# Kernel tuning notes

Hardware: AMD Instinct MI355X
Metric: run time of the kernel (lower is better)

The kernel has to match this reference:

```python
import jax, jax.numpy as jnp
import numpy as np

EPS = 1e-5  # torch LayerNorm default

def _ln(x, g, b):
    mu = jnp.mean(x, -1, keepdims=True)
    var = jnp.mean((x - mu) ** 2, -1, keepdims=True)
    return (x - mu) * jax.lax.rsqrt(var + EPS) * g + b

def _xavier(key, shape):
    fan_in, fan_out = shape[-2], shape[-1]
    s = (2.0 / (fan_in + fan_out)) ** 0.5
    return jax.random.normal(key, shape, dtype=jnp.float32) * s

def setup_inputs() -> dict:
    key = jax.random.key(0)
    ks = jax.random.split(key, 24)
    N, E, B = 10000, 160000, 64
    D, M, FF, K = 128, 32, 32, 5
    EIN = 2 * FF + 1 + 2 * D          # 321
    inp = {}
    inp["coords"] = jax.random.normal(ks[0], (N, 3), dtype=jnp.float32)
    inp["atomids"] = jax.random.randint(ks[1], (N,), 0, 11)
    inp["edge_index"] = jax.random.randint(ks[2], (2, E), 0, N)
    inp["batch"] = jnp.sort(jax.random.randint(ks[3], (N,), 0, B))
    inp["num_graphs"] = B
    inp["emb"] = _xavier(ks[4], (11, D))
    # stacked per-kernel EGNN params (leading dim K=5)
    inp["keW1"] = _xavier(ks[5], (K, EIN, 2 * EIN)); inp["keb1"] = jnp.zeros((K, 2 * EIN))
    inp["keW2"] = _xavier(ks[6], (K, 2 * EIN, M));   inp["keb2"] = jnp.zeros((K, M))
    inp["keng"] = jnp.ones((K, M));   inp["kenb"] = jnp.zeros((K, M))
    inp["kn1g"] = jnp.ones((K, D));   inp["kn1b"] = jnp.zeros((K, D))
    inp["knW1"] = _xavier(ks[7], (K, D + M, 2 * D)); inp["knb1"] = jnp.zeros((K, 2 * D))
    inp["knW2"] = _xavier(ks[8], (K, 2 * D, D));     inp["knb2"] = jnp.zeros((K, D))
    inp["kn2g"] = jnp.ones((K, D));   inp["kn2b"] = jnp.zeros((K, D))
    # fnn: (K+1)*D = 768 -> 256 -> 256 -> 256
    inp["fW0"] = _xavier(ks[9], ((K + 1) * D, 256)); inp["fb0"] = jnp.zeros((256,))
    inp["fW1"] = _xavier(ks[10], (256, 256));        inp["fb1"] = jnp.zeros((256,))
    inp["fW2"] = _xavier(ks[11], (256, 256));        inp["fb2"] = jnp.zeros((256,))
    # fnn2: 256 -> 256 -> 256 -> 1
    inp["gW0"] = _xavier(ks[12], (256, 256));        inp["gb0"] = jnp.zeros((256,))
    inp["gW1"] = _xavier(ks[13], (256, 256));        inp["gb1"] = jnp.zeros((256,))
    inp["gW2"] = _xavier(ks[14], (256, 1));          inp["gb2"] = jnp.zeros((1,))
    return inp

def reference(coords, atomids, edge_index, batch, num_graphs, emb,
              keW1, keb1, keW2, keb2, keng, kenb, kn1g, kn1b,
              knW1, knb1, knW2, knb2, kn2g, kn2b,
              fW0, fb0, fW1, fb1, fW2, fb2,
              gW0, gb0, gW1, gb1, gW2, gb2):
    silu = jax.nn.silu
    N = coords.shape[0]
    src, dst = edge_index[0], edge_index[1]  # x_j = x[src], x_i = x[dst]
    feats = emb[atomids]                                  # [N,128]
    # coords are never updated across kernels -> fourier edge attr computed once
    rel = coords[src] - coords[dst]                       # [E,3]
    d = jnp.sum(rel * rel, -1, keepdims=True)             # [E,1] squared distance
    scales = 2.0 ** jnp.arange(32, dtype=coords.dtype)
    xs = d / scales                                       # [E,32]
    ea = jnp.concatenate([jnp.sin(xs), jnp.cos(xs), d], -1)  # [E,65]
    ones_e = jnp.ones((src.shape[0], 1), feats.dtype)
    deg = jax.ops.segment_sum(ones_e, dst, num_segments=N)   # [N,1]
    deg = jnp.maximum(deg, 1.0)
    feat_list = [feats]
    for k in range(keW1.shape[0]):
        # edge message MLP
        m = jnp.concatenate([feats[dst], feats[src], ea], -1)        # [E,321]
        h = silu(m @ keW1[k] + keb1[k])                              # [E,642]
        m_ij = silu(h @ keW2[k] + keb2[k])                           # [E,32]
        m_ij = _ln(m_ij, keng[k], kenb[k])
        # scatter-mean aggregate to target nodes
        m_i = jax.ops.segment_sum(m_ij, dst, num_segments=N) / deg   # [N,32]
        m_i = _ln(m_i, keng[k], kenb[k])  # (original reuses edge_norm1)
        # node update MLP with residual
        hf = _ln(feats, kn1g[k], kn1b[k])
        h2 = silu(jnp.concatenate([hf, m_i], -1) @ knW1[k] + knb1[k])
        h2 = h2 @ knW2[k] + knb2[k]
        h2 = _ln(h2, kn2g[k], kn2b[k])
        feats = feats + h2
        feat_list.append(feats)
    f = silu(jnp.concatenate(feat_list, -1))              # [N,768]
    f = silu(f @ fW0 + fb0)
    f = silu(f @ fW1 + fb1)
    f = silu(f @ fW2 + fb2)
    gs = jax.ops.segment_sum(f, batch, num_segments=num_graphs)
    gc = jax.ops.segment_sum(jnp.ones((N, 1), f.dtype), batch, num_segments=num_graphs)
    g = gs / jnp.maximum(gc, 1.0)                         # [B,256] scatter_mean
    g = silu(g @ gW0 + gb0)
    g = silu(g @ gW1 + gb1)
    return g @ gW2 + gb2                                  # [B,1]
```

## Files before the change

### kernel.cpp

```cpp
#include <hip/hip_runtime.h>
#include <cstdint>
#include <cstddef>


#define DEV __device__ __forceinline__

typedef __attribute__((ext_vector_type(8))) short bf16x8;
typedef __attribute__((ext_vector_type(4))) float f32x4;

DEV float siluf(float x) { return x / (1.f + __expf(-x)); }

DEV unsigned short f2bf(float f) {
  unsigned u = __float_as_uint(f);
  unsigned r = u + 0x7FFFu + ((u >> 16) & 1u);
  return (unsigned short)(r >> 16);
}
DEV float bf2f(unsigned short h) { return __uint_as_float(((unsigned)h) << 16); }

DEV f32x4 mfma16(bf16x8 a, bf16x8 b, f32x4 c) {
  return __builtin_amdgcn_mfma_f32_16x16x32_bf16(a, b, c, 0, 0, 0);
}

DEV void unpack8(bf16x8 v, float* o) {
#pragma unroll
  for (int j = 0; j < 8; ++j) o[j] = bf2f((unsigned short)v[j]);
}

__global__ __launch_bounds__(256) void k_gather(const int* __restrict__ atomids,
                                                const float* __restrict__ emb,
                                                float* __restrict__ feats_all,
                                                unsigned short* __restrict__ fH, int N) {
  int idx = blockIdx.x * 256 + threadIdx.x;
  if (idx >= N * 128) return;
  int i = idx >> 7, j = idx & 127;
  float v = emb[atomids[i] * 128 + j];
  size_t o = (size_t)i * 768 + j;
  feats_all[o] = v;
  fH[o] = f2bf(v);
}

__global__ __launch_bounds__(256) void k_edge_prep(const float* __restrict__ coords,
                                                   const int* __restrict__ ei, int E,
                                                   float* __restrict__ d_arr,
                                                   int* __restrict__ cnt) {
  int e = blockIdx.x * 256 + threadIdx.x;
  if (e >= E) return;
  int s = ei[e], t = ei[E + e];
  float dx = coords[3 * s + 0] - coords[3 * t + 0];
  float dy = coords[3 * s + 1] - coords[3 * t + 1];
  float dz = coords[3 * s + 2] - coords[3 * t + 2];
  d_arr[e] = dx * dx + dy * dy + dz * dz;
  atomicAdd(&cnt[t], 1);
}

__global__ __launch_bounds__(1024) void k_scan(const int* __restrict__ cnt, int N,
                                               int* __restrict__ cursor,
                                               float* __restrict__ degf) {
  __shared__ int s[1024];
  __shared__ int carry;
  if (threadIdx.x == 0) carry = 0;
  __syncthreads();
  for (int base = 0; base < N; base += 1024) {
    int i = base + threadIdx.x;
    int v = (i < N) ? cnt[i] : 0;
    s[threadIdx.x] = v;
    __syncthreads();
    for (int off = 1; off < 1024; off <<= 1) {
      int add = (threadIdx.x >= off) ? s[threadIdx.x - off] : 0;
      __syncthreads();
      s[threadIdx.x] += add;
      __syncthreads();
    }
    if (i < N) {
      cursor[i] = s[threadIdx.x] - v + carry;
      degf[i] = fmaxf((float)v, 1.f);
    }
    __syncthreads();
    if (threadIdx.x == 0) carry += s[1023];
    __syncthreads();
  }
}

__global__ __launch_bounds__(256) void k_scatter(const int* __restrict__ ei, int E,
                                                 const float* __restrict__ d_arr,
                                                 int* __restrict__ cursor,
                                                 int* __restrict__ ssrc,
                                                 int* __restrict__ sdst,
                                                 float* __restrict__ sd) {
  int e = blockIdx.x * 256 + threadIdx.x;
  if (e >= E) return;
  int s = ei[e], t = ei[E + e];
  int p = atomicAdd(&cursor[t], 1);
  ssrc[p] = s;
  sdst[p] = t;
  sd[p] = d_arr[e];
}

__global__ __launch_bounds__(256) void k_prepack(
    const float* __restrict__ W, size_t wStride, int ldw,
    int K, int Kpad, int Ncols, int Npad,
    unsigned short* __restrict__ hi, unsigned short* __restrict__ lo, size_t oStride) {
  int idx = blockIdx.x * 256 + threadIdx.x;
  int total = Npad * Kpad;
  if (idx >= total) return;
  W += blockIdx.y * wStride;
  hi += blockIdx.y * oStride;
  lo += blockIdx.y * oStride;
  int n = idx / Kpad, k = idx - n * Kpad;
  float v = (n < Ncols && k < K) ? W[(size_t)k * ldw + n] : 0.f;
  unsigned short h = f2bf(v);
  hi[idx] = h;
  lo[idx] = f2bf(v - bf2f(h));
}

__global__ __launch_bounds__(256) void gemm_bf(
    const unsigned short* __restrict__ AH, int lda,
    const unsigned short* __restrict__ BH, const unsigned short* __restrict__ BL, int ldb,
    const float* __restrict__ bias,
    float* __restrict__ C, int ldc,
    unsigned short* __restrict__ CH, int ldch, int outPlaneN,
    int M, int Ncols, int K, int actOut, int actA) {
  const int t = threadIdx.x;
  const int wave = t >> 6, lane = t & 63;
  const int nl = lane & 15, quad = lane >> 4;
  const int bm = blockIdx.x * 128 + wave * 32;
  const int bn = blockIdx.y * 64;
  f32x4 zero = {0.f, 0.f, 0.f, 0.f};
  f32x4 acc[2][4] = {{zero, zero, zero, zero}, {zero, zero, zero, zero}};
  for (int kb = 0; kb < K; kb += 32) {
    bf16x8 ah[2];
#pragma unroll
    for (int h = 0; h < 2; ++h) {
      int row = bm + h * 16 + nl;
      if (row < M) {
        ah[h] = *(const bf16x8*)(AH + (size_t)row * lda + kb + quad * 8);
        if (actA) {
#pragma unroll
          for (int j = 0; j < 8; ++j) {
            float a = siluf(bf2f((unsigned short)ah[h][j]));
            ah[h][j] = (short)f2bf(a);
          }
        }
      } else {
#pragma unroll
        for (int j = 0; j < 8; ++j) ah[h][j] = 0;
      }
    }
#pragma unroll
    for (int tn = 0; tn < 4; ++tn) {
      size_t boff = (size_t)(bn + tn * 16 + nl) * ldb + kb + quad * 8;
      bf16x8 bh = *(const bf16x8*)(BH + boff);
      bf16x8 bl = *(const bf16x8*)(BL + boff);
#pragma unroll
      for (int h = 0; h < 2; ++h) {
        acc[h][tn] = mfma16(ah[h], bh, acc[h][tn]);
        acc[h][tn] = mfma16(ah[h], bl, acc[h][tn]);
      }
    }
  }
#pragma unroll
  for (int h = 0; h < 2; ++h) {
#pragma unroll
    for (int tn = 0; tn < 4; ++tn) {
      int c = bn + tn * 16 + nl;
      float bv = (bias && c < Ncols) ? bias[c] : 0.f;
#pragma unroll
      for (int r = 0; r < 4; ++r) {
        int rr = bm + h * 16 + quad * 4 + r;
        if (rr >= M) continue;
        float v = acc[h][tn][r] + bv;
        if (actOut) v = siluf(v);
        if (C && c < Ncols) C[(size_t)rr * ldc + c] = v;
        if (CH) {
          unsigned short us = f2bf(v);
          if (outPlaneN > 0)
            CH[(size_t)blockIdx.y * outPlaneN + (size_t)rr * 64 + tn * 16 + nl] = us;
          else if (c < Ncols)
            CH[(size_t)rr * ldch + c] = us;
        }
      }
    }
  }
}

__global__ __launch_bounds__(256, 3) void k_edge_mfma(
    const unsigned short* __restrict__ Ap, const unsigned short* __restrict__ Bp,
    int planeN,
    const int* __restrict__ ssrc, const int* __restrict__ sdst,
    const float* __restrict__ sd_g, int E,
    const unsigned short* __restrict__ WeaT,
    const float* __restrict__ Wea64,
    const unsigned short* __restrict__ W2T,
    const float* __restrict__ b2v,
    const float* __restrict__ eng, const float* __restrict__ enb,
    float* __restrict__ msum) {
  __shared__ float sAB[4][16 * 68];
  __shared__ float sH[4][16 * 68];
  __shared__ float sDs[64];
  __shared__ int sSrcS[64], sDstS[64];

  const int t = threadIdx.x;
  const int wave = t >> 6, lane = t & 63;
  const int nl = lane & 15, quad = lane >> 4;
  const int e0 = blockIdx.x * 64;

  if (lane < 16) {
    int el = wave * 16 + lane;
    int e = e0 + el;
    int ec = (e < E) ? e : (E - 1);
    sSrcS[el] = ssrc[ec];
    sDstS[el] = sdst[ec];
    sDs[el] = sd_g[ec];
  }
  const int r = lane >> 2, cq = lane & 3;
  const int elr = wave * 16 + r;
  const size_t aOff = (size_t)sDstS[elr] * 64 + cq * 16;
  const size_t bOff = (size_t)sSrcS[elr] * 64 + cq * 16;
  const float dR = sDs[elr];
  float* myAB = sAB[wave];
  float* myH = sH[wave];

  bf16x8 pa0, pa1, pb0, pb1;
  bf16x8 w1[4][2], w2a[2][2], w2b[2][2];

  auto loadW1 = [&](int c) {
#pragma unroll
    for (int tn = 0; tn < 4; ++tn)
#pragma unroll
      for (int ks = 0; ks < 2; ++ks)
        w1[tn][ks] = *(const bf16x8*)(WeaT + (size_t)(c * 64 + tn * 16 + nl) * 64 +
                                      ks * 32 + quad * 8);
  };
  auto loadW2 = [&](int c, bf16x8(*w)[2]) {
#pragma unroll
    for (int tn = 0; tn < 2; ++tn)
#pragma unroll
      for (int ks = 0; ks < 2; ++ks)
        w[tn][ks] = *(const bf16x8*)(W2T + (size_t)(tn * 16 + nl) * 704 + c * 64 +
                                     ks * 32 + quad * 8);
  };
  auto issue = [&](int c) {
    const unsigned short* a = Ap + (size_t)c * planeN + aOff;
    const unsigned short* b = Bp + (size_t)c * planeN + bOff;
    pa0 = *(const bf16x8*)a;
    pa1 = *(const bf16x8*)(a + 8);
    pb0 = *(const bf16x8*)b;
    pb1 = *(const bf16x8*)(b + 8);
  };
  auto commit = [&](int c) {
    float za[16], zb[16], w[16];
    unpack8(pa0, za); unpack8(pa1, za + 8);
    unpack8(pb0, zb); unpack8(pb1, zb + 8);
    const int cb = c * 64 + cq * 16;
    if (cb + 15 < 642) {
#pragma unroll
      for (int j = 0; j < 4; ++j) {
        f32x4 wv = *(const f32x4*)(Wea64 + cb + 4 * j);
        w[4 * j] = wv.x; w[4 * j + 1] = wv.y; w[4 * j + 2] = wv.z; w[4 * j + 3] = wv.w;
      }
    } else {
#pragma unroll
      for (int u = 0; u < 16; ++u) w[u] = (cb + u < 642) ? Wea64[cb + u] : 0.f;
    }
#pragma unroll
    for (int j = 0; j < 4; ++j) {
      f32x4 o;
#pragma unroll
      for (int u = 0; u < 4; ++u) o[u] = za[4 * j + u] + zb[4 * j + u] + dR * w[4 * j + u];
      *(f32x4*)(myAB + r * 68 + cq * 16 + 4 * j) = o;
    }
  };

  issue(0);
  bf16x8 eaHi[2];
  {
    float d = sDs[wave * 16 + nl];
#pragma unroll
    for (int ks = 0; ks < 2; ++ks)
#pragma unroll
      for (int j = 0; j < 8; ++j) {
        int k = ks * 32 + quad * 8 + j;
        float arg = d * exp2f(-(float)(k & 31));
        float v = (k < 32) ? __sinf(arg) : __cosf(arg);
        eaHi[ks][j] = (short)f2bf(v);
      }
  }
  loadW1(0);
  loadW2(0, w2a);

  f32x4 zero = {0.f, 0.f, 0.f, 0.f};
  f32x4 macc[2] = {zero, zero};

#pragma unroll
  for (int c = 0; c < 11; ++c) {
    commit(c);
    if (c < 10) issue(c + 1);
    f32x4 acc1[4] = {zero, zero, zero, zero};
#pragma unroll
    for (int tn = 0; tn < 4; ++tn)
#pragma unroll
      for (int ks = 0; ks < 2; ++ks) acc1[tn] = mfma16(eaHi[ks], w1[tn][ks], acc1[tn]);
#pragma unroll
    for (int tn = 0; tn < 4; ++tn)
#pragma unroll
      for (int rr = 0; rr < 4; ++rr) {
        int lrow = quad * 4 + rr;
        float z = acc1[tn][rr] + myAB[lrow * 68 + tn * 16 + nl];
        myH[lrow * 68 + tn * 16 + nl] = siluf(z);
      }
    if (c < 10) {
      loadW1(c + 1);
      loadW2(c + 1, (c & 1) ? w2a : w2b);
    }
    bf16x8(*w2)[2] = (c & 1) ? w2b : w2a;
#pragma unroll
    for (int ks = 0; ks < 2; ++ks) {
      f32x4 h0 = *(const f32x4*)(myH + nl * 68 + ks * 32 + quad * 8);
      f32x4 h1 = *(const f32x4*)(myH + nl * 68 + ks * 32 + quad * 8 + 4);
      bf16x8 ah;
      ah[0] = (short)f2bf(h0.x); ah[1] = (short)f2bf(h0.y);
      ah[2] = (short)f2bf(h0.z); ah[3] = (short)f2bf(h0.w);
      ah[4] = (short)f2bf(h1.x); ah[5] = (short)f2bf(h1.y);
      ah[6] = (short)f2bf(h1.z); ah[7] = (short)f2bf(h1.w);
#pragma unroll
      for (int tn = 0; tn < 2; ++tn) macc[tn] = mfma16(ah, w2[tn][ks], macc[tn]);
    }
  }

  float g0 = eng[nl], g1v = eng[16 + nl], bb0 = enb[nl], bb1 = enb[16 + nl];
  float bi0 = b2v[nl], bi1 = b2v[16 + nl];
  float* sMw = myH;
#pragma unroll
  for (int rr = 0; rr < 4; ++rr) {
    float v0 = siluf(macc[0][rr] + bi0);
    float v1 = siluf(macc[1][rr] + bi1);
    float s = v0 + v1;
    float ss = v0 * v0 + v1 * v1;
#pragma unroll
    for (int m = 1; m < 16; m <<= 1) {
      s += __shfl_xor(s, m, 16);
      ss += __shfl_xor(ss, m, 16);
    }
    float mu = s * (1.f / 32.f);
    float var = ss * (1.f / 32.f) - mu * mu;
    float rs = rsqrtf(var + 1e-5f);
    int lr = quad * 4 + rr;
    sMw[lr * 33 + nl] = (v0 - mu) * rs * g0 + bb0;
    sMw[lr * 33 + 16 + nl] = (v1 - mu) * rs * g1v + bb1;
  }
  __syncthreads();
  {
    int col = t & 31, seg = t >> 5;
    float acc = 0.f;
    int cur = -1;
#pragma unroll
    for (int i = 0; i < 8; ++i) {
      int e = seg * 8 + i;
      int dn = (e0 + e < E) ? sDstS[e] : -1;
      if (dn != cur) {
        if (cur >= 0) atomicAdd(&msum[(size_t)cur * 32 + col], acc);
        acc = 0.f;
        cur = dn;
      }
      if (dn >= 0) acc += sH[e >> 4][(e & 15) * 33 + col];
    }
    if (cur >= 0) atomicAdd(&msum[(size_t)cur * 32 + col], acc);
  }
}

__global__ __launch_bounds__(256) void k_node_ln(
    const float* __restrict__ msum, const float* __restrict__ deg,
    const float* __restrict__ featsAll, int k,
    const float* __restrict__ n1g, const float* __restrict__ n1b,
    const float* __restrict__ eng, const float* __restrict__ enb,
    unsigned short* __restrict__ hcatH, int N) {
  int node = blockIdx.x * 4 + (threadIdx.x >> 6);
  int lane = threadIdx.x & 63;
  if (node >= N) return;
  const float* fr = featsAll + (size_t)node * 768 + k * 128;
  float x0 = fr[lane], x1 = fr[64 + lane];
  float s = x0 + x1;
#pragma unroll
  for (int m = 1; m < 64; m <<= 1) s += __shfl_xor(s, m, 64);
  float mu = s * (1.f / 128.f);
  float d0 = x0 - mu, d1 = x1 - mu;
  float v = d0 * d0 + d1 * d1;
#pragma unroll
  for (int m = 1; m < 64; m <<= 1) v += __shfl_xor(v, m, 64);
  float rstd = rsqrtf(v * (1.f / 128.f) + 1e-5f);
  size_t hb = (size_t)node * 160;
  hcatH[hb + lane] = f2bf(d0 * rstd * n1g[lane] + n1b[lane]);
  hcatH[hb + 64 + lane] = f2bf(d1 * rstd * n1g[64 + lane] + n1b[64 + lane]);
  float dg = deg[node];
  int col = lane & 31;
  float y = msum[(size_t)node * 32 + col] / dg;
  float sy = y;
#pragma unroll
  for (int m = 1; m < 32; m <<= 1) sy += __shfl_xor(sy, m, 32);
  float mu2 = sy * (1.f / 32.f);
  float dy = y - mu2;
  float vy = dy * dy;
#pragma unroll
  for (int m = 1; m < 32; m <<= 1) vy += __shfl_xor(vy, m, 32);
  float rstd2 = rsqrtf(vy * (1.f / 32.f) + 1e-5f);
  if (lane < 32) hcatH[hb + 128 + col] = f2bf(dy * rstd2 * eng[col] + enb[col]);
}

__global__ __launch_bounds__(256) void k_node_resid(
    const float* __restrict__ t2, float* __restrict__ featsAll, int k,
    const float* __restrict__ n2g, const float* __restrict__ n2b,
    unsigned short* __restrict__ fH, int N) {
  int node = blockIdx.x * 4 + (threadIdx.x >> 6);
  int lane = threadIdx.x & 63;
  if (node >= N) return;
  const float* tr = t2 + (size_t)node * 128;
  float x0 = tr[lane], x1 = tr[64 + lane];
  float s = x0 + x1;
#pragma unroll
  for (int m = 1; m < 64; m <<= 1) s += __shfl_xor(s, m, 64);
  float mu = s * (1.f / 128.f);
  float d0 = x0 - mu, d1 = x1 - mu;
  float v = d0 * d0 + d1 * d1;
#pragma unroll
  for (int m = 1; m < 64; m <<= 1) v += __shfl_xor(v, m, 64);
  float rstd = rsqrtf(v * (1.f / 128.f) + 1e-5f);
  const float* fk = featsAll + (size_t)node * 768 + k * 128;
  size_t ob = (size_t)node * 768 + (k + 1) * 128;
  float o0 = fk[lane] + d0 * rstd * n2g[lane] + n2b[lane];
  float o1 = fk[64 + lane] + d1 * rstd * n2g[64 + lane] + n2b[64 + lane];
  featsAll[ob + lane] = o0;
  featsAll[ob + 64 + lane] = o1;
  fH[ob + lane] = f2bf(o0);
  fH[ob + 64 + lane] = f2bf(o1);
}

__global__ __launch_bounds__(256) void k_pool2(const float* __restrict__ f,
                                               const int* __restrict__ batch,
                                               float* __restrict__ gsum,
                                               float* __restrict__ gcnt, int N) {
  int n0 = blockIdx.x * 64;
  int col = threadIdx.x;
  float acc = 0.f;
  int cur = -1;
  for (int i = 0; i < 64; ++i) {
    int n = n0 + i;
    if (n >= N) break;
    int b = batch[n];
    if (b != cur) {
      if (cur >= 0) atomicAdd(&gsum[cur * 256 + col], acc);
      acc = 0.f;
      cur = b;
    }
    acc += f[(size_t)n * 256 + col];
  }
  if (cur >= 0) atomicAdd(&gsum[cur * 256 + col], acc);
  if (threadIdx.x == 0) {
    int cnt = 0;
    cur = -1;
    for (int i = 0; i < 64; ++i) {
      int n = n0 + i;
      if (n >= N) break;
      int b = batch[n];
      if (b != cur) {
        if (cur >= 0) atomicAdd(&gcnt[cur], (float)cnt);
        cnt = 0;
        cur = b;
      }
      cnt++;
    }
    if (cur >= 0) atomicAdd(&gcnt[cur], (float)cnt);
  }
}

__global__ void k_gdiv(float* gsum, const float* gcnt, unsigned short* gH) {
  int b = blockIdx.x, j = threadIdx.x;
  float v = gsum[b * 256 + j] / fmaxf(gcnt[b], 1.f);
  gH[b * 256 + j] = f2bf(v);
}

__global__ void k_gout(const float* __restrict__ g2, const float* __restrict__ gW2,
                       const float* __restrict__ gb2, float* __restrict__ out) {
  int b = threadIdx.x;
  if (b >= 64) return;
  float s = gb2[0];
  for (int j = 0; j < 256; ++j) s += g2[b * 256 + j] * gW2[j];
  out[b] = s;
}

extern "C" void kernel_launch(void* const* d_in, const int* in_sizes, int n_in,
                              void* d_out, int out_size, void* d_ws, size_t ws_size,
                              hipStream_t stream) {
  const float* coords = (const float*)d_in[0];
  const int* atomids = (const int*)d_in[1];
  const int* ei = (const int*)d_in[2];
  const int* batch = (const int*)d_in[3];
  const float* emb = (const float*)d_in[5];
  const float* keW1 = (const float*)d_in[6];
  const float* keb1 = (const float*)d_in[7];
  const float* keW2 = (const float*)d_in[8];
  const float* keb2 = (const float*)d_in[9];
  const float* keng = (const float*)d_in[10];
  const float* kenb = (const float*)d_in[11];
  const float* kn1g = (const float*)d_in[12];
  const float* kn1b = (const float*)d_in[13];
  const float* knW1 = (const float*)d_in[14];
  const float* knb1 = (const float*)d_in[15];
  const float* knW2 = (const float*)d_in[16];
  const float* knb2 = (const float*)d_in[17];
  const float* kn2g = (const float*)d_in[18];
  const float* kn2b = (const float*)d_in[19];
  const float* fW0 = (const float*)d_in[20];
  const float* fb0 = (const float*)d_in[21];
  const float* fW1 = (const float*)d_in[22];
  const float* fb1 = (const float*)d_in[23];
  const float* fW2 = (const float*)d_in[24];
  const float* fb2 = (const float*)d_in[25];
  const float* gW0 = (const float*)d_in[26];
  const float* gb0 = (const float*)d_in[27];
  const float* gW1 = (const float*)d_in[28];
  const float* gb1 = (const float*)d_in[29];
  const float* gW2 = (const float*)d_in[30];
  const float* gb2 = (const float*)d_in[31];

  const int N = in_sizes[0] / 3;
  const int E = in_sizes[2] / 2;
  const int planeN = N * 64;

  size_t off = 0;
  auto alloc = [&](size_t n) {
    float* p = (float*)d_ws + off;
    off += (n + 63) & ~(size_t)63;
    return p;
  };
  float* feats_all = alloc((size_t)N * 768);
  float* d_arr = alloc(E);
  float* degf = alloc(N);
  float* msum = alloc((size_t)N * 32);
  float* t2 = alloc((size_t)N * 128);
  float* f1 = alloc((size_t)N * 256);
  float* gsum = alloc(64 * 256);
  float* gcnt = alloc(64);
  float* g2 = alloc(64 * 256);
  int* cnt = (int*)alloc(N);
  int* cursor = (int*)alloc(N);
  int* ssrc = (int*)alloc(E);
  int* sdst = (int*)alloc(E);
  float* sd = alloc(E);

  unsigned short* ubase = (unsigned short*)(alloc(0));
  size_t uoff = 0;
  auto ualloc = [&](size_t n) {
    unsigned short* p = ubase + uoff;
    uoff += (n + 63) & ~(size_t)63;
    return p;
  };
  unsigned short* fH = ualloc((size_t)N * 768);
  unsigned short* ApU = ualloc((size_t)11 * planeN);
  unsigned short* BpU = ualloc((size_t)11 * planeN);
  unsigned short* hcatH = ualloc((size_t)N * 160);
  unsigned short* t1H = ualloc((size_t)N * 256);
  unsigned short* fAH = ualloc((size_t)N * 256);
  unsigned short* fBH = ualloc((size_t)N * 256);
  unsigned short* gH = ualloc(64 * 256);
  unsigned short* g1H = ualloc(64 * 256);
  const size_t sDst_ = 704 * 128, sSrc_ = 704 * 128, sEa_ = 704 * 64;
  const size_t sW2_ = 32 * 704, sN1_ = 256 * 160, sN2_ = 128 * 256;
  unsigned short* PdstH = ualloc(5 * sDst_); unsigned short* PdstL = ualloc(5 * sDst_);
  unsigned short* PsrcH = ualloc(5 * sSrc_); unsigned short* PsrcL = ualloc(5 * sSrc_);
  unsigned short* PeaH = ualloc(5 * sEa_);   unsigned short* PeaL = ualloc(5 * sEa_);
  unsigned short* PW2H = ualloc(5 * sW2_);   unsigned short* PW2L = ualloc(5 * sW2_);
  unsigned short* Pn1H = ualloc(5 * sN1_);   unsigned short* Pn1L = ualloc(5 * sN1_);
  unsigned short* Pn2H = ualloc(5 * sN2_);   unsigned short* Pn2L = ualloc(5 * sN2_);
  unsigned short* Pf0H = ualloc(256 * 768);  unsigned short* Pf0L = ualloc(256 * 768);
  unsigned short* Pf1H = ualloc(256 * 256);  unsigned short* Pf1L = ualloc(256 * 256);
  unsigned short* Pf2H = ualloc(256 * 256);  unsigned short* Pf2L = ualloc(256 * 256);
  unsigned short* Pg0H = ualloc(256 * 256);  unsigned short* Pg0L = ualloc(256 * 256);
  unsigned short* Pg1H = ualloc(256 * 256);  unsigned short* Pg1L = ualloc(256 * 256);

  auto pp = [&](const float* W, size_t wStr, int ldw, int K, int Kpad, int Nc, int Npad,
                unsigned short* hi, unsigned short* lo, size_t oStr, int layers) {
    int total = Npad * Kpad;
    k_prepack<<<dim3((total + 255) / 256, layers), 256, 0, stream>>>(
        W, wStr, ldw, K, Kpad, Nc, Npad, hi, lo, oStr);
  };
  pp(keW1, (size_t)321 * 642, 642, 128, 128, 642, 704, PdstH, PdstL, sDst_, 5);
  pp(keW1 + 128 * 642, (size_t)321 * 642, 642, 128, 128, 642, 704, PsrcH, PsrcL, sSrc_, 5);
  pp(keW1 + 256 * 642, (size_t)321 * 642, 642, 64, 64, 642, 704, PeaH, PeaL, sEa_, 5);
  pp(keW2, (size_t)642 * 32, 32, 642, 704, 32, 32, PW2H, PW2L, sW2_, 5);
  pp(knW1, (size_t)160 * 256, 256, 160, 160, 256, 256, Pn1H, Pn1L, sN1_, 5);
  pp(knW2, (size_t)256 * 128, 128, 256, 256, 128, 128, Pn2H, Pn2L, sN2_, 5);
  pp(fW0, 0, 256, 768, 768, 256, 256, Pf0H, Pf0L, 0, 1);
  pp(fW1, 0, 256, 256, 256, 256, 256, Pf1H, Pf1L, 0, 1);
  pp(fW2, 0, 256, 256, 256, 256, 256, Pf2H, Pf2L, 0, 1);
  pp(gW0, 0, 256, 256, 256, 256, 256, Pg0H, Pg0L, 0, 1);
  pp(gW1, 0, 256, 256, 256, 256, 256, Pg1H, Pg1L, 0, 1);

  k_gather<<<(N * 128 + 255) / 256, 256, 0, stream>>>(atomids, emb, feats_all, fH, N);
  hipMemsetAsync(cnt, 0, (size_t)N * sizeof(int), stream);
  k_edge_prep<<<(E + 255) / 256, 256, 0, stream>>>(coords, ei, E, d_arr, cnt);
  k_scan<<<1, 1024, 0, stream>>>(cnt, N, cursor, degf);
  k_scatter<<<(E + 255) / 256, 256, 0, stream>>>(ei, E, d_arr, cursor, ssrc, sdst, sd);

  const int MT = (N + 127) / 128;
  for (int k = 0; k < 5; ++k) {
    gemm_bf<<<dim3(MT, 11), 256, 0, stream>>>(
        fH + k * 128, 768, PdstH + k * sDst_, PdstL + k * sDst_, 128,
        keb1 + k * 642, nullptr, 0, ApU, 0, planeN, N, 642, 128, 0, 0);
    gemm_bf<<<dim3(MT, 11), 256, 0, stream>>>(
        fH + k * 128, 768, PsrcH + k * sSrc_, PsrcL + k * sSrc_, 128,
        nullptr, nullptr, 0, BpU, 0, planeN, N, 642, 128, 0, 0);
    hipMemsetAsync(msum, 0, (size_t)N * 32 * sizeof(float), stream);
    k_edge_mfma<<<(E + 63) / 64, 256, 0, stream>>>(
        ApU, BpU, planeN, ssrc, sdst, sd, E,
        PeaH + k * sEa_,
        keW1 + (size_t)k * 321 * 642 + (size_t)320 * 642,
        PW2H + k * sW2_,
        keb2 + k * 32, keng + k * 32, kenb + k * 32, msum);
    k_node_ln<<<(N + 3) / 4, 256, 0, stream>>>(
        msum, degf, feats_all, k, kn1g + k * 128, kn1b + k * 128,
        keng + k * 32, kenb + k * 32, hcatH, N);
    gemm_bf<<<dim3(MT, 4), 256, 0, stream>>>(
        hcatH, 160, Pn1H + k * sN1_, Pn1L + k * sN1_, 160,
        knb1 + k * 256, nullptr, 0, t1H, 256, 0, N, 256, 160, 1, 0);
    gemm_bf<<<dim3(MT, 2), 256, 0, stream>>>(
        t1H, 256, Pn2H + k * sN2_, Pn2L + k * sN2_, 256,
        knb2 + k * 128, t2, 128, nullptr, 0, 0, N, 128, 256, 0, 0);
    k_node_resid<<<(N + 3) / 4, 256, 0, stream>>>(
        t2, feats_all, k, kn2g + k * 128, kn2b + k * 128, fH, N);
  }

  gemm_bf<<<dim3(MT, 4), 256, 0, stream>>>(
      fH, 768, Pf0H, Pf0L, 768, fb0, nullptr, 0, fAH, 256, 0, N, 256, 768, 1, 1);
  gemm_bf<<<dim3(MT, 4), 256, 0, stream>>>(
      fAH, 256, Pf1H, Pf1L, 256, fb1, nullptr, 0, fBH, 256, 0, N, 256, 256, 1, 0);
  gemm_bf<<<dim3(MT, 4), 256, 0, stream>>>(
      fBH, 256, Pf2H, Pf2L, 256, fb2, f1, 256, nullptr, 0, 0, N, 256, 256, 1, 0);

  hipMemsetAsync(gsum, 0, 64 * 256 * sizeof(float), stream);
  hipMemsetAsync(gcnt, 0, 64 * sizeof(float), stream);
  k_pool2<<<(N + 63) / 64, 256, 0, stream>>>(f1, batch, gsum, gcnt, N);
  k_gdiv<<<64, 256, 0, stream>>>(gsum, gcnt, gH);
  gemm_bf<<<dim3(1, 4), 256, 0, stream>>>(
      gH, 256, Pg0H, Pg0L, 256, gb0, nullptr, 0, g1H, 256, 0, 64, 256, 256, 1, 0);
  gemm_bf<<<dim3(1, 4), 256, 0, stream>>>(
      g1H, 256, Pg1H, Pg1L, 256, gb1, g2, 256, nullptr, 0, 0, 64, 256, 256, 1, 0);
  k_gout<<<1, 64, 0, stream>>>(g2, gW2, gb2, (float*)d_out);
}
```

Baseline: 1.868 ms.

## Merge dst/src projection GEMMs and slim edge kernel registers and LDS

```diff
diff --git a/kernel.cpp b/kernel.cpp
--- a/kernel.cpp
+++ b/kernel.cpp
@@ -118,7 +118,7 @@
     const unsigned short* __restrict__ BH, const unsigned short* __restrict__ BL, int ldb,
     const float* __restrict__ bias,
     float* __restrict__ C, int ldc,
-    unsigned short* __restrict__ CH, int ldch, int outPlaneN,
+    unsigned short* __restrict__ CH, int ldch,
     int M, int Ncols, int K, int actOut, int actA) {
   const int t = threadIdx.x;
   const int wave = t >> 6, lane = t & 63;
@@ -171,19 +171,75 @@
         float v = acc[h][tn][r] + bv;
         if (actOut) v = siluf(v);
         if (C && c < Ncols) C[(size_t)rr * ldc + c] = v;
-        if (CH) {
-          unsigned short us = f2bf(v);
-          if (outPlaneN > 0)
-            CH[(size_t)blockIdx.y * outPlaneN + (size_t)rr * 64 + tn * 16 + nl] = us;
-          else if (c < Ncols)
-            CH[(size_t)rr * ldch + c] = us;
-        }
-      }
-    }
-  }
-}
-
-__global__ __launch_bounds__(256, 3) void k_edge_mfma(
+        if (CH && c < Ncols) CH[(size_t)rr * ldch + c] = f2bf(v);
+      }
+    }
+  }
+}
+
+__global__ __launch_bounds__(256) void gemm_proj(
+    const unsigned short* __restrict__ AH, int lda,
+    const unsigned short* __restrict__ B1H, const unsigned short* __restrict__ B1L,
+    const unsigned short* __restrict__ B2H, const unsigned short* __restrict__ B2L,
+    const float* __restrict__ bias1,
+    unsigned short* __restrict__ C1, unsigned short* __restrict__ C2,
+    int planeN, int M) {
+  const int y = blockIdx.y;
+  const unsigned short* BH;
+  const unsigned short* BL;
+  const float* bias;
+  unsigned short* CP;
+  int yp;
+  if (y < 11) { BH = B1H; BL = B1L; bias = bias1; CP = C1; yp = y; }
+  else        { BH = B2H; BL = B2L; bias = nullptr; CP = C2; yp = y - 11; }
+  const int t = threadIdx.x;
+  const int wave = t >> 6, lane = t & 63;
+  const int nl = lane & 15, quad = lane >> 4;
+  const int bm = blockIdx.x * 128 + wave * 32;
+  const int bn = yp * 64;
+  f32x4 zero = {0.f, 0.f, 0.f, 0.f};
+  f32x4 acc[2][4] = {{zero, zero, zero, zero}, {zero, zero, zero, zero}};
+  for (int kb = 0; kb < 128; kb += 32) {
+    bf16x8 ah[2];
+#pragma unroll
+    for (int h = 0; h < 2; ++h) {
+      int row = bm + h * 16 + nl;
+      if (row < M)
+        ah[h] = *(const bf16x8*)(AH + (size_t)row * lda + kb + quad * 8);
+      else
+#pragma unroll
+        for (int j = 0; j < 8; ++j) ah[h][j] = 0;
+    }
+#pragma unroll
+    for (int tn = 0; tn < 4; ++tn) {
+      size_t boff = (size_t)(bn + tn * 16 + nl) * 128 + kb + quad * 8;
+      bf16x8 bh = *(const bf16x8*)(BH + boff);
+      bf16x8 bl = *(const bf16x8*)(BL + boff);
+#pragma unroll
+      for (int h = 0; h < 2; ++h) {
+        acc[h][tn] = mfma16(ah[h], bh, acc[h][tn]);
+        acc[h][tn] = mfma16(ah[h], bl, acc[h][tn]);
+      }
+    }
+  }
+#pragma unroll
+  for (int h = 0; h < 2; ++h) {
+#pragma unroll
+    for (int tn = 0; tn < 4; ++tn) {
+      int c = bn + tn * 16 + nl;
+      float bv = (bias && c < 642) ? bias[c] : 0.f;
+#pragma unroll
+      for (int r = 0; r < 4; ++r) {
+        int rr = bm + h * 16 + quad * 4 + r;
+        if (rr >= M) continue;
+        CP[(size_t)yp * planeN + (size_t)rr * 64 + tn * 16 + nl] =
+            f2bf(acc[h][tn][r] + bv);
+      }
+    }
+  }
+}
+
+__global__ __launch_bounds__(256, 4) void k_edge_mfma(
     const unsigned short* __restrict__ Ap, const unsigned short* __restrict__ Bp,
     int planeN,
     const int* __restrict__ ssrc, const int* __restrict__ sdst,
@@ -195,7 +251,7 @@
     const float* __restrict__ eng, const float* __restrict__ enb,
     float* __restrict__ msum) {
   __shared__ float sAB[4][16 * 68];
-  __shared__ float sH[4][16 * 68];
+  __shared__ unsigned short sHh[4][16 * 72];
   __shared__ float sDs[64];
   __shared__ int sSrcS[64], sDstS[64];
 
@@ -218,10 +274,10 @@
   const size_t bOff = (size_t)sSrcS[elr] * 64 + cq * 16;
   const float dR = sDs[elr];
   float* myAB = sAB[wave];
-  float* myH = sH[wave];
+  unsigned short* myH = sHh[wave];
 
   bf16x8 pa0, pa1, pb0, pb1;
-  bf16x8 w1[4][2], w2a[2][2], w2b[2][2];
+  bf16x8 w1[4][2], w2[2][2];
 
   auto loadW1 = [&](int c) {
 #pragma unroll
@@ -231,13 +287,13 @@
         w1[tn][ks] = *(const bf16x8*)(WeaT + (size_t)(c * 64 + tn * 16 + nl) * 64 +
                                       ks * 32 + quad * 8);
   };
-  auto loadW2 = [&](int c, bf16x8(*w)[2]) {
+  auto loadW2 = [&](int c) {
 #pragma unroll
     for (int tn = 0; tn < 2; ++tn)
 #pragma unroll
       for (int ks = 0; ks < 2; ++ks)
-        w[tn][ks] = *(const bf16x8*)(W2T + (size_t)(tn * 16 + nl) * 704 + c * 64 +
-                                     ks * 32 + quad * 8);
+        w2[tn][ks] = *(const bf16x8*)(W2T + (size_t)(tn * 16 + nl) * 704 + c * 64 +
+                                      ks * 32 + quad * 8);
   };
   auto issue = [&](int c) {
     const unsigned short* a = Ap + (size_t)c * planeN + aOff;
@@ -286,50 +342,42 @@
       }
   }
   loadW1(0);
-  loadW2(0, w2a);
+  loadW2(0);
 
   f32x4 zero = {0.f, 0.f, 0.f, 0.f};
   f32x4 macc[2] = {zero, zero};
 
-#pragma unroll
   for (int c = 0; c < 11; ++c) {
     commit(c);
     if (c < 10) issue(c + 1);
-    f32x4 acc1[4] = {zero, zero, zero, zero};
+    f32x4 acc1[4];
 #pragma unroll
     for (int tn = 0; tn < 4; ++tn)
 #pragma unroll
+      for (int rr = 0; rr < 4; ++rr)
+        acc1[tn][rr] = myAB[(quad * 4 + rr) * 68 + tn * 16 + nl];
+#pragma unroll
+    for (int tn = 0; tn < 4; ++tn)
+#pragma unroll
       for (int ks = 0; ks < 2; ++ks) acc1[tn] = mfma16(eaHi[ks], w1[tn][ks], acc1[tn]);
+    if (c < 10) loadW1(c + 1);
 #pragma unroll
     for (int tn = 0; tn < 4; ++tn)
 #pragma unroll
-      for (int rr = 0; rr < 4; ++rr) {
-        int lrow = quad * 4 + rr;
-        float z = acc1[tn][rr] + myAB[lrow * 68 + tn * 16 + nl];
-        myH[lrow * 68 + tn * 16 + nl] = siluf(z);
-      }
-    if (c < 10) {
-      loadW1(c + 1);
-      loadW2(c + 1, (c & 1) ? w2a : w2b);
-    }
-    bf16x8(*w2)[2] = (c & 1) ? w2b : w2a;
+      for (int rr = 0; rr < 4; ++rr)
+        myH[(quad * 4 + rr) * 72 + tn * 16 + nl] = f2bf(siluf(acc1[tn][rr]));
 #pragma unroll
     for (int ks = 0; ks < 2; ++ks) {
-      f32x4 h0 = *(const f32x4*)(myH + nl * 68 + ks * 32 + quad * 8);
-      f32x4 h1 = *(const f32x4*)(myH + nl * 68 + ks * 32 + quad * 8 + 4);
-      bf16x8 ah;
-      ah[0] = (short)f2bf(h0.x); ah[1] = (short)f2bf(h0.y);
-      ah[2] = (short)f2bf(h0.z); ah[3] = (short)f2bf(h0.w);
-      ah[4] = (short)f2bf(h1.x); ah[5] = (short)f2bf(h1.y);
-      ah[6] = (short)f2bf(h1.z); ah[7] = (short)f2bf(h1.w);
+      bf16x8 ah = *(const bf16x8*)(myH + nl * 72 + ks * 32 + quad * 8);
 #pragma unroll
       for (int tn = 0; tn < 2; ++tn) macc[tn] = mfma16(ah, w2[tn][ks], macc[tn]);
     }
+    if (c < 10) loadW2(c + 1);
   }
 
   float g0 = eng[nl], g1v = eng[16 + nl], bb0 = enb[nl], bb1 = enb[16 + nl];
   float bi0 = b2v[nl], bi1 = b2v[16 + nl];
-  float* sMw = myH;
+  float* sMw = myAB;
 #pragma unroll
   for (int rr = 0; rr < 4; ++rr) {
     float v0 = siluf(macc[0][rr] + bi0);
@@ -362,7 +410,7 @@
         acc = 0.f;
         cur = dn;
       }
-      if (dn >= 0) acc += sH[e >> 4][(e & 15) * 33 + col];
+      if (dn >= 0) acc += sAB[e >> 4][(e & 15) * 33 + col];
     }
     if (cur >= 0) atomicAdd(&msum[(size_t)cur * 32 + col], acc);
   }
@@ -603,12 +651,11 @@
 
   const int MT = (N + 127) / 128;
   for (int k = 0; k < 5; ++k) {
-    gemm_bf<<<dim3(MT, 11), 256, 0, stream>>>(
-        fH + k * 128, 768, PdstH + k * sDst_, PdstL + k * sDst_, 128,
-        keb1 + k * 642, nullptr, 0, ApU, 0, planeN, N, 642, 128, 0, 0);
-    gemm_bf<<<dim3(MT, 11), 256, 0, stream>>>(
-        fH + k * 128, 768, PsrcH + k * sSrc_, PsrcL + k * sSrc_, 128,
-        nullptr, nullptr, 0, BpU, 0, planeN, N, 642, 128, 0, 0);
+    gemm_proj<<<dim3(MT, 22), 256, 0, stream>>>(
+        fH + k * 128, 768,
+        PdstH + k * sDst_, PdstL + k * sDst_,
+        PsrcH + k * sSrc_, PsrcL + k * sSrc_,
+        keb1 + k * 642, ApU, BpU, planeN, N);
     hipMemsetAsync(msum, 0, (size_t)N * 32 * sizeof(float), stream);
     k_edge_mfma<<<(E + 63) / 64, 256, 0, stream>>>(
         ApU, BpU, planeN, ssrc, sdst, sd, E,
@@ -621,28 +668,28 @@
         keng + k * 32, kenb + k * 32, hcatH, N);
     gemm_bf<<<dim3(MT, 4), 256, 0, stream>>>(
         hcatH, 160, Pn1H + k * sN1_, Pn1L + k * sN1_, 160,
-        knb1 + k * 256, nullptr, 0, t1H, 256, 0, N, 256, 160, 1, 0);
+        knb1 + k * 256, nullptr, 0, t1H, 256, N, 256, 160, 1, 0);
     gemm_bf<<<dim3(MT, 2), 256, 0, stream>>>(
         t1H, 256, Pn2H + k * sN2_, Pn2L + k * sN2_, 256,
-        knb2 + k * 128, t2, 128, nullptr, 0, 0, N, 128, 256, 0, 0);
+        knb2 + k * 128, t2, 128, nullptr, 0, N, 128, 256, 0, 0);
     k_node_resid<<<(N + 3) / 4, 256, 0, stream>>>(
         t2, feats_all, k, kn2g + k * 128, kn2b + k * 128, fH, N);
   }
 
   gemm_bf<<<dim3(MT, 4), 256, 0, stream>>>(
-      fH, 768, Pf0H, Pf0L, 768, fb0, nullptr, 0, fAH, 256, 0, N, 256, 768, 1, 1);
+      fH, 768, Pf0H, Pf0L, 768, fb0, nullptr, 0, fAH, 256, N, 256, 768, 1, 1);
   gemm_bf<<<dim3(MT, 4), 256, 0, stream>>>(
-      fAH, 256, Pf1H, Pf1L, 256, fb1, nullptr, 0, fBH, 256, 0, N, 256, 256, 1, 0);
+      fAH, 256, Pf1H, Pf1L, 256, fb1, nullptr, 0, fBH, 256, N, 256, 256, 1, 0);
   gemm_bf<<<dim3(MT, 4), 256, 0, stream>>>(
-      fBH, 256, Pf2H, Pf2L, 256, fb2, f1, 256, nullptr, 0, 0, N, 256, 256, 1, 0);
+      fBH, 256, Pf2H, Pf2L, 256, fb2, f1, 256, nullptr, 0, N, 256, 256, 1, 0);
 
   hipMemsetAsync(gsum, 0, 64 * 256 * sizeof(float), stream);
   hipMemsetAsync(gcnt, 0, 64 * sizeof(float), stream);
   k_pool2<<<(N + 63) / 64, 256, 0, stream>>>(f1, batch, gsum, gcnt, N);
   k_gdiv<<<64, 256, 0, stream>>>(gsum, gcnt, gH);
   gemm_bf<<<dim3(1, 4), 256, 0, stream>>>(
-      gH, 256, Pg0H, Pg0L, 256, gb0, nullptr, 0, g1H, 256, 0, 64, 256, 256, 1, 0);
+      gH, 256, Pg0H, Pg0L, 256, gb0, nullptr, 0, g1H, 256, 64, 256, 256, 1, 0);
   gemm_bf<<<dim3(1, 4), 256, 0, stream>>>(
-      g1H, 256, Pg1H, Pg1L, 256, gb1, g2, 256, nullptr, 0, 0, 64, 256, 256, 1, 0);
+      g1H, 256, Pg1H, Pg1L, 256, gb1, g2, 256, nullptr, 0, 64, 256, 256, 1, 0);
   k_gout<<<1, 64, 0, stream>>>(g2, gW2, gb2, (float*)d_out);
 }
```

Result: slower. 1.928 ms (+3.2%).
